# Performance work log

Hardware: AMD Instinct MI355X
Metric: run time of the kernel (lower is better)

## Reference

```python
import jax, jax.numpy as jnp
import numpy as np
import math

S, D, H = 2048, 1024, 16
HS = D // H

def setup_inputs() -> dict:
    key = jax.random.key(0)
    ks = jax.random.split(key, 3)
    return {
        "hidden_states": jax.random.normal(ks[0], (S, D), dtype=jnp.float32),
        "W_attn": jax.random.normal(ks[1], (D, 3 * D), dtype=jnp.float32) * 0.02,
        "b_attn": jnp.zeros((3 * D,), dtype=jnp.float32),
        "W_proj": jax.random.normal(ks[2], (D, D), dtype=jnp.float32) * 0.02,
        "b_proj": jnp.zeros((D,), dtype=jnp.float32),
    }

def reference(hidden_states, W_attn, b_attn, W_proj, b_proj):
    s, d = hidden_states.shape
    qkv = hidden_states @ W_attn + b_attn  # [S, 3D]
    q, k, v = jnp.split(qkv, 3, axis=1)
    split = lambda x: x.reshape(s, H, HS).transpose(1, 0, 2)  # [H, S, HS]
    q, k, v = split(q), split(k), split(v)
    # NOTE: source scales by sqrt(key_length), not sqrt(head_size)
    att = jnp.einsum('hqd,hkd->hqk', q, k, precision='highest') / math.sqrt(s)
    mask = jnp.tril(jnp.ones((s, s), dtype=bool))  # causal
    att = jnp.where(mask, att, jnp.finfo(att.dtype).min)
    att = jax.nn.softmax(att, axis=-1)
    out = jnp.einsum('hqk,hkd->hqd', att, v, precision='highest')
    out = out.transpose(1, 0, 2).reshape(s, d)  # merge heads
    return out @ W_proj + b_proj
```

## Files before the change

kernel.cpp:

```cpp
#include <hip/hip_runtime.h>
#include <cstdint>


typedef __bf16 bf16;
typedef __attribute__((ext_vector_type(4))) float f32x4;
typedef __attribute__((ext_vector_type(8))) bf16 bf16x8;
typedef __attribute__((ext_vector_type(4))) bf16 bf16x4;

#define S_LEN 2048
#define D_DIM 1024
#define NH 16
#define HS 64
#define CHUNK 8
#define NCK 4

__device__ __forceinline__ bf16 f2bf(float f) {
  uint32_t u = __builtin_bit_cast(uint32_t, f);
  uint32_t r = (u + 0x7FFFu + ((u >> 16) & 1u)) >> 16;
  unsigned short s = (unsigned short)r;
  return __builtin_bit_cast(bf16, s);
}

__device__ __forceinline__ void load_lds16(const void* g, void* l) {
  __builtin_amdgcn_global_load_lds(
      (__attribute__((address_space(1))) unsigned int*)(uintptr_t)g,
      (__attribute__((address_space(3))) unsigned int*)l, 16, 0, 0);
}

__device__ __forceinline__ uint32_t pack_bf16(float lo, float hi) {
  uint32_t a = __builtin_bit_cast(uint32_t, lo) + 0x8000u;
  uint32_t b = __builtin_bit_cast(uint32_t, hi) + 0x8000u;
  return __builtin_amdgcn_perm(b, a, 0x07060302u);
}

__global__ __launch_bounds__(256) void prep_kernel(
    const float* __restrict__ hs, const float* __restrict__ Wa,
    const float* __restrict__ Wp, bf16* __restrict__ hsb,
    bf16* __restrict__ WaT, bf16* __restrict__ WpT) {
  const int bid = blockIdx.x;
  if (bid < 2048) {
    const int i = bid * 256 + threadIdx.x;
    float4 v = ((const float4*)hs)[i];
    bf16x4 o;
    o[0] = f2bf(v.x); o[1] = f2bf(v.y); o[2] = f2bf(v.z); o[3] = f2bf(v.w);
    ((bf16x4*)hsb)[i] = o;
    return;
  }
  __shared__ float tile[32][33];
  const int tb = bid - 2048;
  const int bx = tb & 127;
  const int r0 = (tb >> 7) * 32;
  const bool isA = bx < 96;
  const float* in = isA ? Wa : Wp;
  bf16* out = isA ? WaT : WpT;
  const int C = isA ? 3072 : 1024;
  const int c0 = (isA ? bx : bx - 96) * 32;
  const int x = threadIdx.x & 31, y = threadIdx.x >> 5;
  for (int k = 0; k < 32; k += 8)
    tile[y + k][x] = in[(size_t)(r0 + y + k) * C + c0 + x];
  __syncthreads();
  for (int k = 0; k < 32; k += 8)
    out[(size_t)(c0 + y + k) * 1024 + r0 + x] = f2bf(tile[x][y + k]);
}

template <int BM, int BN, int MODE>
__global__ __launch_bounds__(256) void gemm_bt_kernel(
    const bf16* __restrict__ A, const bf16* __restrict__ Bt,
    const float* __restrict__ bias, void* __restrict__ Cout,
    bf16* __restrict__ VtOut, int M, int N, int K) {
  constexpr int MI = (BN == 128) ? 4 : (BM == 128 ? 2 : 1);
  constexpr int NI = 4;
  __shared__ bf16 As[BM * 32];
  __shared__ bf16 Bs[BN * 32];
  const int t = threadIdx.x;
  const int wave = t >> 6;
  const int lane = t & 63;
  const int quad = lane >> 4;
  const int l16 = lane & 15;
  const int m0 = blockIdx.y * BM;
  const int n0 = blockIdx.x * BN;
  const int wm = (BN == 128) ? (wave >> 1) * 64
                             : (BM == 128 ? wave * 32 : wave * 16);
  const int wn = (BN == 128) ? (wave & 1) * 64 : 0;

  f32x4 acc[MI][NI];
  for (int i = 0; i < MI; i++)
    for (int j = 0; j < NI; j++)
      for (int r = 0; r < 4; r++) acc[i][j][r] = 0.f;

  const int srow = t >> 2;
  const int scol = (t & 3) * 8;
  const bf16* Ag = A + (size_t)(m0 + srow) * K + scol;
  const bf16* Bg = Bt + (size_t)(n0 + srow) * K + scol;
  bf16* Asl = As + t * 8;
  bf16* Bsl = Bs + t * 8;

  for (int k0 = 0; k0 < K; k0 += 32) {
    __syncthreads();
    for (int r = 0; r < BM; r += 64)
      load_lds16(Ag + (size_t)r * K + k0, Asl + r * 32);
    for (int r = 0; r < BN; r += 64)
      load_lds16(Bg + (size_t)r * K + k0, Bsl + r * 32);
    __syncthreads();
    bf16x8 af[MI], bfr[NI];
    for (int i = 0; i < MI; i++)
      af[i] = *(const bf16x8*)(As + (wm + i * 16 + l16) * 32 + quad * 8);
    for (int i = 0; i < NI; i++)
      bfr[i] = *(const bf16x8*)(Bs + (wn + i * 16 + l16) * 32 + quad * 8);
    for (int mi = 0; mi < MI; mi++)
      for (int ni = 0; ni < NI; ni++)
        acc[mi][ni] = __builtin_amdgcn_mfma_f32_16x16x32_bf16(
            af[mi], bfr[ni], acc[mi][ni], 0, 0, 0);
  }

  const bool isV = (MODE == 2) && (n0 >= 2 * D_DIM);
  for (int mi = 0; mi < MI; mi++) {
    for (int ni = 0; ni < NI; ni++) {
      const int col = n0 + wn + ni * 16 + l16;
      const float bv = bias ? bias[col] : 0.0f;
      const int row0 = m0 + wm + mi * 16 + quad * 4;
      if (isV) {
        uint32_t w0 = pack_bf16(acc[mi][ni][0] + bv, acc[mi][ni][1] + bv);
        uint32_t w1 = pack_bf16(acc[mi][ni][2] + bv, acc[mi][ni][3] + bv);
        uint2 wv; wv.x = w0; wv.y = w1;
        *(uint2*)(VtOut + (size_t)(col - 2 * D_DIM) * S_LEN + row0) = wv;
      } else {
        for (int r = 0; r < 4; r++) {
          float v = acc[mi][ni][r] + bv;
          if (MODE == 0)
            ((float*)Cout)[(size_t)(row0 + r) * N + col] = v;
          else
            ((bf16*)Cout)[(size_t)(row0 + r) * N + col] = f2bf(v);
        }
      }
    }
  }
}

__global__ __launch_bounds__(256) void attn_kernel(
    const bf16* __restrict__ qkv, const bf16* __restrict__ Vt,
    bf16* __restrict__ Opart, float* __restrict__ ml) {
  __shared__ bf16 Qs[128 * 64];
  __shared__ bf16 Ks[2][64 * 64];
  __shared__ bf16 Vs[2][64 * 64];

  const int t = threadIdx.x;
  const int wave = t >> 6;
  const int lane = t & 63;
  const int quad = lane >> 4;
  const int l16 = lane & 15;
  const int h = blockIdx.x & 15;
  const int rank = blockIdx.x >> 4;
  int qt = 15, c = 0;
  {
    int acc = 0;
    for (int q = 15; q >= 0; q--) {
      const int n = (q >> 2) + 1;
      if (rank < acc + n) { qt = q; c = rank - acc; break; }
      acc += n;
    }
  }
  const int kt0 = c * CHUNK;
  const int kt1 = min(kt0 + CHUNK, 2 * qt + 2);
  const float SC = 0.022097086912079608f;

  const int srow = t >> 3;
  const int gcol = (((t & 7) ^ (srow & 7))) * 8;

  for (int j = 0; j < 4; j++)
    load_lds16(
        qkv + (size_t)(qt * 128 + j * 32 + srow) * (3 * D_DIM) + h * HS + gcol,
        Qs + j * 2048 + t * 8);

  auto issueKV = [&](int kt, int b) {
    const bf16* gk =
        qkv + (size_t)(kt * 64 + srow) * (3 * D_DIM) + D_DIM + h * HS + gcol;
    load_lds16(gk, Ks[b] + t * 8);
    load_lds16(gk + (size_t)32 * (3 * D_DIM), Ks[b] + t * 8 + 32 * 64);
    const bf16* gv = Vt + (size_t)(h * HS + srow) * S_LEN + kt * 64 + gcol;
    load_lds16(gv, Vs[b] + t * 8);
    load_lds16(gv + (size_t)32 * S_LEN, Vs[b] + t * 8 + 32 * 64);
  };
  issueKV(kt0, 0);
  __syncthreads();

  const int px = (quad ^ (l16 & 7)) * 8;
  bf16x8 bq[2][2];
  int Qb[2], qglob[2];
  for (int sq = 0; sq < 2; sq++) {
    const int qr = (2 * wave + sq) * 16 + l16;
    bq[sq][0] = *(const bf16x8*)(Qs + qr * 64 + px);
    bq[sq][1] = *(const bf16x8*)(Qs + qr * 64 + (px ^ 32));
    Qb[sq] = qt * 128 + (2 * wave + sq) * 16;
    qglob[sq] = Qb[sq] + l16;
  }

  int bpidx[4];
  for (int dw = 0; dw < 4; dw++)
    bpidx[dw] = ((((quad & 1) * 2 + (dw >> 1)) * 16 + l16) << 2);
  const bool sel_hi = (quad >> 1) != 0;

  float l_i[2] = {0.f, 0.f};
  f32x4 o[2][4];
  for (int sq = 0; sq < 2; sq++)
    for (int dt = 0; dt < 4; dt++)
      for (int r = 0; r < 4; r++) o[sq][dt][r] = 0.f;

  for (int kt = kt0; kt < kt1; kt++) {
    const int b = (kt - kt0) & 1;
    if (kt > kt0) __syncthreads();
    if (kt + 1 < kt1) issueKV(kt + 1, b ^ 1);

    f32x4 st[2][4];
    for (int sq = 0; sq < 2; sq++)
      for (int nt = 0; nt < 4; nt++)
        for (int r = 0; r < 4; r++) st[sq][nt][r] = 0.f;
    for (int nt = 0; nt < 4; nt++) {
      bf16x8 ak0 = *(const bf16x8*)(Ks[b] + (nt * 16 + l16) * 64 + px);
      bf16x8 ak1 = *(const bf16x8*)(Ks[b] + (nt * 16 + l16) * 64 + (px ^ 32));
      for (int sq = 0; sq < 2; sq++) {
        st[sq][nt] =
            __builtin_amdgcn_mfma_f32_16x16x32_bf16(ak0, bq[sq][0], st[sq][nt], 0, 0, 0);
        st[sq][nt] =
            __builtin_amdgcn_mfma_f32_16x16x32_bf16(ak1, bq[sq][1], st[sq][nt], 0, 0, 0);
      }
    }

    uint32_t pk[2][4][2];
    float rs[2] = {0.f, 0.f};
    for (int sq = 0; sq < 2; sq++) {
      float p[4][4];
      if (kt * 64 + 63 > Qb[sq]) {
        for (int nt = 0; nt < 4; nt++)
          for (int r = 0; r < 4; r++) {
            const int key = kt * 64 + nt * 16 + quad * 4 + r;
            p[nt][r] = (key <= qglob[sq]) ? __expf(st[sq][nt][r] * SC) : 0.f;
          }
      } else {
        for (int nt = 0; nt < 4; nt++)
          for (int r = 0; r < 4; r++) p[nt][r] = __expf(st[sq][nt][r] * SC);
      }
      for (int nt = 0; nt < 4; nt++)
        for (int r = 0; r < 4; r++) rs[sq] += p[nt][r];
      for (int nt = 0; nt < 4; nt++) {
        pk[sq][nt][0] = pack_bf16(p[nt][0], p[nt][1]);
        pk[sq][nt][1] = pack_bf16(p[nt][2], p[nt][3]);
      }
    }
    for (int sq = 0; sq < 2; sq++) {
      rs[sq] += __shfl_xor(rs[sq], 16, 64);
      rs[sq] += __shfl_xor(rs[sq], 32, 64);
      l_i[sq] += rs[sq];
    }

    for (int half = 0; half < 2; half++) {
      bf16x8 bpv[2];
      for (int sq = 0; sq < 2; sq++) {
        uint32_t dwv[4];
        for (int dw = 0; dw < 4; dw++) {
          int f0 = __builtin_amdgcn_ds_bpermute(bpidx[dw],
                                                (int)pk[sq][half * 2 + 0][dw & 1]);
          int f1 = __builtin_amdgcn_ds_bpermute(bpidx[dw],
                                                (int)pk[sq][half * 2 + 1][dw & 1]);
          dwv[dw] = (uint32_t)(sel_hi ? f1 : f0);
        }
        union { uint32_t u[4]; bf16x8 v; } u_;
        u_.u[0] = dwv[0]; u_.u[1] = dwv[1]; u_.u[2] = dwv[2]; u_.u[3] = dwv[3];
        bpv[sq] = u_.v;
      }
      const int vpx = half ? (px ^ 32) : px;
      for (int dt = 0; dt < 4; dt++) {
        bf16x8 av = *(const bf16x8*)(Vs[b] + (dt * 16 + l16) * 64 + vpx);
        o[0][dt] = __builtin_amdgcn_mfma_f32_16x16x32_bf16(av, bpv[0], o[0][dt], 0, 0, 0);
        o[1][dt] = __builtin_amdgcn_mfma_f32_16x16x32_bf16(av, bpv[1], o[1][dt], 0, 0, 0);
      }
    }
  }

  for (int sq = 0; sq < 2; sq++) {
    const float inv_l = 1.0f / l_i[sq];
    const int qrow = Qb[sq] + l16;
    const size_t pbase = (((size_t)c * NH + h) * S_LEN + qrow) * 64;
    for (int dt = 0; dt < 4; dt++) {
      uint32_t w0 = pack_bf16(o[sq][dt][0] * inv_l, o[sq][dt][1] * inv_l);
      uint32_t w1 = pack_bf16(o[sq][dt][2] * inv_l, o[sq][dt][3] * inv_l);
      uint2 wv; wv.x = w0; wv.y = w1;
      *(uint2*)(Opart + pbase + dt * 16 + quad * 4) = wv;
    }
    if (quad == 0) ml[((size_t)c * NH + h) * S_LEN + qrow] = l_i[sq];
  }
}

__global__ __launch_bounds__(256) void combine_kernel(
    const bf16* __restrict__ Opart, const float* __restrict__ ml,
    bf16* __restrict__ Obf) {
  const int wave = threadIdx.x >> 6;
  const int lane = threadIdx.x & 63;
  const int idx = blockIdx.x * 4 + wave;
  const int h = idx >> 11;
  const int qrow = idx & 2047;
  const int nc = (qrow >> 6) / CHUNK + 1;

  float aw = 0.f, ao = 0.f;
  for (int cix = 0; cix < nc; cix++) {
    const float w = ml[((size_t)cix * NH + h) * S_LEN + qrow];
    aw += w;
    ao += w * (float)Opart[(((size_t)cix * NH + h) * S_LEN + qrow) * 64 + lane];
  }
  Obf[(size_t)qrow * D_DIM + h * HS + lane] = f2bf(ao / aw);
}

extern "C" void kernel_launch(void* const* d_in, const int* in_sizes, int n_in,
                              void* d_out, int out_size, void* d_ws,
                              size_t ws_size, hipStream_t stream) {
  const float* hs = (const float*)d_in[0];
  const float* Wa = (const float*)d_in[1];
  const float* ba = (const float*)d_in[2];
  const float* Wp = (const float*)d_in[3];
  const float* bp = (const float*)d_in[4];
  float* out = (float*)d_out;

  char* ws = (char*)d_ws;
  bf16* hsb   = (bf16*)(ws);
  bf16* WaT   = (bf16*)(ws + (4ull << 20));
  bf16* WpT   = (bf16*)(ws + (10ull << 20));
  bf16* qkv   = (bf16*)(ws + (12ull << 20));
  bf16* Vt    = (bf16*)(ws + (24ull << 20));
  bf16* Obf   = (bf16*)(ws + (28ull << 20));
  bf16* Opart = (bf16*)(ws + (32ull << 20));
  float* mlp  = (float*)(ws + (48ull << 20));

  prep_kernel<<<6144, 256, 0, stream>>>(hs, Wa, Wp, hsb, WaT, WpT);
  gemm_bt_kernel<128, 64, 2><<<dim3(3 * D_DIM / 64, S_LEN / 128), 256, 0,
                               stream>>>(hsb, WaT, ba, qkv, Vt, S_LEN,
                                         3 * D_DIM, D_DIM);
  attn_kernel<<<640, 256, 0, stream>>>(qkv, Vt, Opart, mlp);
  combine_kernel<<<(S_LEN * NH) / 4, 256, 0, stream>>>(Opart, mlp, Obf);
  gemm_bt_kernel<64, 64, 0><<<dim3(D_DIM / 64, S_LEN / 64), 256, 0, stream>>>(
      Obf, WpT, bp, out, nullptr, S_LEN, D_DIM, D_DIM);

  (void)in_sizes; (void)n_in; (void)out_size; (void)ws_size;
}
```

Baseline: 153.5 us.

## Widen GEMM K-tile with swizzled LDS, enlarge tiles, compute row sums via MFMA

```diff
diff --git a/kernel.cpp b/kernel.cpp
--- a/kernel.cpp
+++ b/kernel.cpp
@@ -68,10 +68,10 @@
     const bf16* __restrict__ A, const bf16* __restrict__ Bt,
     const float* __restrict__ bias, void* __restrict__ Cout,
     bf16* __restrict__ VtOut, int M, int N, int K) {
-  constexpr int MI = (BN == 128) ? 4 : (BM == 128 ? 2 : 1);
+  constexpr int MI = (BN == 128) ? 4 : 2;
   constexpr int NI = 4;
-  __shared__ bf16 As[BM * 32];
-  __shared__ bf16 Bs[BN * 32];
+  __shared__ bf16 As[BM * 64];
+  __shared__ bf16 Bs[BN * 64];
   const int t = threadIdx.x;
   const int wave = t >> 6;
   const int lane = t & 63;
@@ -79,8 +79,7 @@
   const int l16 = lane & 15;
   const int m0 = blockIdx.y * BM;
   const int n0 = blockIdx.x * BN;
-  const int wm = (BN == 128) ? (wave >> 1) * 64
-                             : (BM == 128 ? wave * 32 : wave * 16);
+  const int wm = (BN == 128) ? (wave >> 1) * 64 : wave * 32;
   const int wn = (BN == 128) ? (wave & 1) * 64 : 0;
 
   f32x4 acc[MI][NI];
@@ -88,29 +87,33 @@
     for (int j = 0; j < NI; j++)
       for (int r = 0; r < 4; r++) acc[i][j][r] = 0.f;
 
-  const int srow = t >> 2;
-  const int scol = (t & 3) * 8;
-  const bf16* Ag = A + (size_t)(m0 + srow) * K + scol;
-  const bf16* Bg = Bt + (size_t)(n0 + srow) * K + scol;
-  bf16* Asl = As + t * 8;
-  bf16* Bsl = Bs + t * 8;
-
-  for (int k0 = 0; k0 < K; k0 += 32) {
+  const int srow = t >> 3;
+  const int gcol = ((t & 7) ^ (srow & 7)) * 8;
+  const bf16* Ag = A + (size_t)(m0 + srow) * K + gcol;
+  const bf16* Bg = Bt + (size_t)(n0 + srow) * K + gcol;
+
+  const int fx0 = ((0 * 4 + quad) ^ (l16 & 7)) * 8;
+  const int fx1 = ((1 * 4 + quad) ^ (l16 & 7)) * 8;
+
+  for (int k0 = 0; k0 < K; k0 += 64) {
     __syncthreads();
-    for (int r = 0; r < BM; r += 64)
-      load_lds16(Ag + (size_t)r * K + k0, Asl + r * 32);
-    for (int r = 0; r < BN; r += 64)
-      load_lds16(Bg + (size_t)r * K + k0, Bsl + r * 32);
+    for (int j = 0; j < BM / 32; j++)
+      load_lds16(Ag + (size_t)(j * 32) * K + k0, As + j * 2048 + t * 8);
+    for (int j = 0; j < BN / 32; j++)
+      load_lds16(Bg + (size_t)(j * 32) * K + k0, Bs + j * 2048 + t * 8);
     __syncthreads();
-    bf16x8 af[MI], bfr[NI];
-    for (int i = 0; i < MI; i++)
-      af[i] = *(const bf16x8*)(As + (wm + i * 16 + l16) * 32 + quad * 8);
-    for (int i = 0; i < NI; i++)
-      bfr[i] = *(const bf16x8*)(Bs + (wn + i * 16 + l16) * 32 + quad * 8);
-    for (int mi = 0; mi < MI; mi++)
-      for (int ni = 0; ni < NI; ni++)
-        acc[mi][ni] = __builtin_amdgcn_mfma_f32_16x16x32_bf16(
-            af[mi], bfr[ni], acc[mi][ni], 0, 0, 0);
+    for (int kh = 0; kh < 2; kh++) {
+      const int fx = kh ? fx1 : fx0;
+      bf16x8 af[MI], bfr[NI];
+      for (int i = 0; i < MI; i++)
+        af[i] = *(const bf16x8*)(As + (wm + i * 16 + l16) * 64 + fx);
+      for (int i = 0; i < NI; i++)
+        bfr[i] = *(const bf16x8*)(Bs + (wn + i * 16 + l16) * 64 + fx);
+      for (int mi = 0; mi < MI; mi++)
+        for (int ni = 0; ni < NI; ni++)
+          acc[mi][ni] = __builtin_amdgcn_mfma_f32_16x16x32_bf16(
+              af[mi], bfr[ni], acc[mi][ni], 0, 0, 0);
+    }
   }
 
   const bool isV = (MODE == 2) && (n0 >= 2 * D_DIM);
@@ -200,11 +203,16 @@
     bpidx[dw] = ((((quad & 1) * 2 + (dw >> 1)) * 16 + l16) << 2);
   const bool sel_hi = (quad >> 1) != 0;
 
-  float l_i[2] = {0.f, 0.f};
-  f32x4 o[2][4];
-  for (int sq = 0; sq < 2; sq++)
+  const bf16 one_bf = f2bf(1.0f);
+  const bf16x8 ones = {one_bf, one_bf, one_bf, one_bf,
+                       one_bf, one_bf, one_bf, one_bf};
+
+  f32x4 o[2][4], ol[2];
+  for (int sq = 0; sq < 2; sq++) {
     for (int dt = 0; dt < 4; dt++)
       for (int r = 0; r < 4; r++) o[sq][dt][r] = 0.f;
+    for (int r = 0; r < 4; r++) ol[sq][r] = 0.f;
+  }
 
   for (int kt = kt0; kt < kt1; kt++) {
     const int b = (kt - kt0) & 1;
@@ -227,7 +235,6 @@
     }
 
     uint32_t pk[2][4][2];
-    float rs[2] = {0.f, 0.f};
     for (int sq = 0; sq < 2; sq++) {
       float p[4][4];
       if (kt * 64 + 63 > Qb[sq]) {
@@ -240,17 +247,10 @@
         for (int nt = 0; nt < 4; nt++)
           for (int r = 0; r < 4; r++) p[nt][r] = __expf(st[sq][nt][r] * SC);
       }
-      for (int nt = 0; nt < 4; nt++)
-        for (int r = 0; r < 4; r++) rs[sq] += p[nt][r];
       for (int nt = 0; nt < 4; nt++) {
         pk[sq][nt][0] = pack_bf16(p[nt][0], p[nt][1]);
         pk[sq][nt][1] = pack_bf16(p[nt][2], p[nt][3]);
       }
-    }
-    for (int sq = 0; sq < 2; sq++) {
-      rs[sq] += __shfl_xor(rs[sq], 16, 64);
-      rs[sq] += __shfl_xor(rs[sq], 32, 64);
-      l_i[sq] += rs[sq];
     }
 
     for (int half = 0; half < 2; half++) {
@@ -274,11 +274,14 @@
         o[0][dt] = __builtin_amdgcn_mfma_f32_16x16x32_bf16(av, bpv[0], o[0][dt], 0, 0, 0);
         o[1][dt] = __builtin_amdgcn_mfma_f32_16x16x32_bf16(av, bpv[1], o[1][dt], 0, 0, 0);
       }
+      ol[0] = __builtin_amdgcn_mfma_f32_16x16x32_bf16(ones, bpv[0], ol[0], 0, 0, 0);
+      ol[1] = __builtin_amdgcn_mfma_f32_16x16x32_bf16(ones, bpv[1], ol[1], 0, 0, 0);
     }
   }
 
   for (int sq = 0; sq < 2; sq++) {
-    const float inv_l = 1.0f / l_i[sq];
+    const float l_v = ol[sq][0];
+    const float inv_l = 1.0f / l_v;
     const int qrow = Qb[sq] + l16;
     const size_t pbase = (((size_t)c * NH + h) * S_LEN + qrow) * 64;
     for (int dt = 0; dt < 4; dt++) {
@@ -287,7 +290,7 @@
       uint2 wv; wv.x = w0; wv.y = w1;
       *(uint2*)(Opart + pbase + dt * 16 + quad * 4) = wv;
     }
-    if (quad == 0) ml[((size_t)c * NH + h) * S_LEN + qrow] = l_i[sq];
+    if (quad == 0) ml[((size_t)c * NH + h) * S_LEN + qrow] = l_v;
   }
 }
 
@@ -331,12 +334,12 @@
   float* mlp  = (float*)(ws + (48ull << 20));
 
   prep_kernel<<<6144, 256, 0, stream>>>(hs, Wa, Wp, hsb, WaT, WpT);
-  gemm_bt_kernel<128, 64, 2><<<dim3(3 * D_DIM / 64, S_LEN / 128), 256, 0,
-                               stream>>>(hsb, WaT, ba, qkv, Vt, S_LEN,
-                                         3 * D_DIM, D_DIM);
+  gemm_bt_kernel<128, 128, 2><<<dim3(3 * D_DIM / 128, S_LEN / 128), 256, 0,
+                                stream>>>(hsb, WaT, ba, qkv, Vt, S_LEN,
+                                          3 * D_DIM, D_DIM);
   attn_kernel<<<640, 256, 0, stream>>>(qkv, Vt, Opart, mlp);
   combine_kernel<<<(S_LEN * NH) / 4, 256, 0, stream>>>(Opart, mlp, Obf);
-  gemm_bt_kernel<64, 64, 0><<<dim3(D_DIM / 64, S_LEN / 64), 256, 0, stream>>>(
+  gemm_bt_kernel<128, 64, 0><<<dim3(D_DIM / 64, S_LEN / 128), 256, 0, stream>>>(
       Obf, WpT, bp, out, nullptr, S_LEN, D_DIM, D_DIM);
 
   (void)in_sizes; (void)n_in; (void)out_size; (void)ws_size;
```

After: 154.0 us. About the same (+0.3%).
